# Kernel optimization log

Measured on AMD Instinct MI355X. Metric: run time of the kernel, lower is better.

Reference implementation:

```python
import jax, jax.numpy as jnp
import numpy as np

HIDDEN = 1024
HEADS = 16
HEAD_DIM = HIDDEN // HEADS  # 64
B, S = 4, 2048


def setup_inputs() -> dict:
    key = jax.random.key(0)
    ks = jax.random.split(key, 8)
    scale = 1.0 / np.sqrt(HIDDEN)
    return {
        "hidden_states": jax.random.normal(ks[0], (B, S, HIDDEN), dtype=jnp.float32),
        "attention_mask": jnp.zeros((B, S), dtype=jnp.float32),  # additive mask: 0 = keep
        "Wq": jax.random.normal(ks[1], (HIDDEN, HIDDEN), dtype=jnp.float32) * scale,
        "bq": jnp.zeros((HIDDEN,), dtype=jnp.float32),
        "Wk": jax.random.normal(ks[2], (HIDDEN, HIDDEN), dtype=jnp.float32) * scale,
        "bk": jnp.zeros((HIDDEN,), dtype=jnp.float32),
        "Wv": jax.random.normal(ks[3], (HIDDEN, HIDDEN), dtype=jnp.float32) * scale,
        "bv": jnp.zeros((HIDDEN,), dtype=jnp.float32),
    }


def reference(hidden_states, attention_mask, Wq, bq, Wk, bk, Wv, bv):
    b, s, _ = hidden_states.shape

    def split_heads(x):  # [b,s,hidden] -> [b,h,s,d]
        return x.reshape(b, s, HEADS, HEAD_DIM).transpose(0, 2, 1, 3)

    q = split_heads(hidden_states @ Wq + bq)
    k = split_heads(hidden_states @ Wk + bk)
    v = split_heads(hidden_states @ Wv + bv)

    # [b,h,s,s] attention scores, scaled, with additive mask broadcast to [b,1,1,s]
    scores = jnp.einsum("bhqd,bhkd->bhqk", q, k) / np.sqrt(HEAD_DIM)
    scores = scores + attention_mask[:, None, None, :]
    probs = jax.nn.softmax(scores, axis=-1)
    # dropout prob = 0 (eval); head_mask=None
    ctx = jnp.einsum("bhqk,bhkd->bhqd", probs, v)  # [b,h,s,d]
    return ctx.transpose(0, 2, 1, 3).reshape(b, s, HIDDEN)
```

## Files before the change

### kernel.cpp

```cpp
#include <hip/hip_runtime.h>
#include <hip/hip_bf16.h>

typedef unsigned short u16t;
typedef unsigned int   u32t;
typedef float  f32x4  __attribute__((ext_vector_type(4)));
typedef __bf16 bf16x8 __attribute__((ext_vector_type(8)));

#define HIDDEN 1024
#define HEADS  16
#define HDIM   64
#define BB     4
#define SS     2048
#define BH     (BB * HEADS)
#define MTOT   (BB * SS)

__device__ inline u16t f2bf(float f) {
  __hip_bfloat16 h = __float2bfloat16(f);
  return *reinterpret_cast<u16t*>(&h);
}

__device__ inline void gload_lds16(const void* g, void* l) {
  __builtin_amdgcn_global_load_lds(
      (const __attribute__((address_space(1))) void*)g,
      (__attribute__((address_space(3))) void*)l, 16, 0, 0);
}

__global__ __launch_bounds__(256) void k_convert_x(const float* __restrict__ X,
                                                   u16t* __restrict__ Xb, int n4) {
  int i = blockIdx.x * blockDim.x + threadIdx.x;
  int stride = gridDim.x * blockDim.x;
  for (; i < n4; i += stride) {
    float4 v = reinterpret_cast<const float4*>(X)[i];
    ushort4 o;
    o.x = f2bf(v.x); o.y = f2bf(v.y); o.z = f2bf(v.z); o.w = f2bf(v.w);
    reinterpret_cast<ushort4*>(Xb)[i] = o;
  }
}

__global__ __launch_bounds__(256) void k_transpose_w(const float* __restrict__ Wq,
                                                     const float* __restrict__ Wk,
                                                     const float* __restrict__ Wv,
                                                     u16t* __restrict__ Wt) {
  __shared__ float tile[64][65];
  const int mat = blockIdx.z;
  const float* W = (mat == 0) ? Wq : (mat == 1) ? Wk : Wv;
  const int k0 = blockIdx.x * 64, n0 = blockIdx.y * 64;
  const int t = threadIdx.x;
  const int c = t & 63, rbase = t >> 6;
#pragma unroll
  for (int p = 0; p < 16; ++p) {
    int r = p * 4 + rbase;
    tile[r][c] = W[(size_t)(k0 + r) * HIDDEN + n0 + c];
  }
  __syncthreads();
  u16t* Wo = Wt + (size_t)mat * HIDDEN * HIDDEN;
#pragma unroll
  for (int p = 0; p < 16; ++p) {
    int r = p * 4 + rbase;
    Wo[(size_t)(n0 + r) * HIDDEN + k0 + c] = f2bf(tile[c][r]);
  }
}

__global__ __launch_bounds__(256) void k_qkv_gemm(const u16t* __restrict__ Xb,
                                                  const u16t* __restrict__ Wt,
                                                  const float* __restrict__ bq,
                                                  const float* __restrict__ bk,
                                                  const float* __restrict__ bv,
                                                  u16t* __restrict__ QKV) {
  __shared__ __align__(16) u16t As[128 * 64];
  __shared__ __align__(16) u16t Bs[128 * 64];
  const int m0 = blockIdx.x * 128, n0 = blockIdx.y * 128;
  const int tid = threadIdx.x;
  const int w = tid >> 6, l = tid & 63;
  const int lq = l & 15, g = l >> 4;
  const int wm = (w >> 1) * 64, wn = (w & 1) * 64;

  f32x4 acc[4][4] = {};

  for (int t = 0; t < 16; ++t) {
    const int k0 = t * 64;
    __syncthreads();
#pragma unroll
    for (int p = 0; p < 4; ++p) {
      int chunk = p * 256 + tid;
      int row = chunk >> 3, c16 = chunk & 7;
      int sc = ((c16 ^ (row & 7)) * 8);
      gload_lds16(Xb + (size_t)(m0 + row) * HIDDEN + k0 + sc,
                  &As[(p * 256 + w * 64) * 8]);
      gload_lds16(Wt + (size_t)(n0 + row) * HIDDEN + k0 + sc,
                  &Bs[(p * 256 + w * 64) * 8]);
    }
    __syncthreads();
#pragma unroll
    for (int kc = 0; kc < 2; ++kc) {
      bf16x8 af[4], bfr[4];
#pragma unroll
      for (int i = 0; i < 4; ++i) {
        int rowA = wm + i * 16 + lq;
        af[i] = *reinterpret_cast<const bf16x8*>(
            &As[rowA * 64 + (((kc * 4 + g) ^ (rowA & 7)) * 8)]);
        int rowB = wn + i * 16 + lq;
        bfr[i] = *reinterpret_cast<const bf16x8*>(
            &Bs[rowB * 64 + (((kc * 4 + g) ^ (rowB & 7)) * 8)]);
      }
#pragma unroll
      for (int i = 0; i < 4; ++i)
#pragma unroll
        for (int j = 0; j < 4; ++j)
          acc[i][j] = __builtin_amdgcn_mfma_f32_16x16x32_bf16(af[i], bfr[j],
                                                              acc[i][j], 0, 0, 0);
    }
  }

  const int nb = n0 >> 10;
  const float* bias = (nb == 0) ? bq : (nb == 1) ? bk : bv;
  const float scl = (nb == 0) ? 0.125f : 1.0f;
#pragma unroll
  for (int j = 0; j < 4; ++j) {
    int n = (n0 & 1023) + wn + j * 16 + lq;
    int h = n >> 6, d = n & 63;
    float bval = bias[n];
#pragma unroll
    for (int i = 0; i < 4; ++i) {
#pragma unroll
      for (int r = 0; r < 4; ++r) {
        int m = m0 + wm + i * 16 + g * 4 + r;
        int b = m >> 11, s = m & 2047;
        QKV[(((size_t)(nb * BH + b * HEADS + h)) * SS + s) * HDIM + d] =
            f2bf((acc[i][j][r] + bval) * scl);
      }
    }
  }
}

__global__ __launch_bounds__(256) void k_attn(const u16t* __restrict__ QKV,
                                              const float* __restrict__ mask,
                                              float* __restrict__ out) {
  __shared__ __align__(16) u16t Ks[64 * 64];
  __shared__ __align__(16) u16t Vt[64 * 64];
  const int qt = blockIdx.x, bh = blockIdx.y;
  const int b = bh >> 4, h = bh & 15;
  const int tid = threadIdx.x, w = tid >> 6, l = tid & 63;
  const int lq = l & 15, g = l >> 4;
  const int q0 = qt * 128 + w * 32;

  const u16t* Qh = QKV + (size_t)bh * SS * HDIM;
  const u16t* Kh = QKV + (size_t)(BH + bh) * SS * HDIM;
  const u16t* Vh = QKV + (size_t)(2 * BH + bh) * SS * HDIM;

  bf16x8 qf[2][2];
#pragma unroll
  for (int qi = 0; qi < 2; ++qi) {
    qf[qi][0] = *reinterpret_cast<const bf16x8*>(
        &Qh[(size_t)(q0 + qi * 16 + lq) * HDIM + g * 8]);
    qf[qi][1] = *reinterpret_cast<const bf16x8*>(
        &Qh[(size_t)(q0 + qi * 16 + lq) * HDIM + 32 + g * 8]);
  }

  float m_run[2] = {-1e30f, -1e30f};
  float lsum[2] = {0.f, 0.f};
  f32x4 ctx[2][4] = {};

  const int srcl1 = ((2 * g) & 3) * 16 + lq;
  const int srcl2 = ((2 * g + 1) & 3) * 16 + lq;
  const bool hi = (g >= 2);

  for (int kv = 0; kv < 32; ++kv) {
    const int k0 = kv * 64;
    __syncthreads();
#pragma unroll
    for (int p = 0; p < 2; ++p) {
      int chunk = p * 256 + tid;
      int row = chunk >> 3, c16 = chunk & 7;
      gload_lds16(Kh + (size_t)(k0 + row) * HDIM + ((c16 ^ (row & 7)) * 8),
                  &Ks[(p * 256 + w * 64) * 8]);
    }
#pragma unroll
    for (int p = 0; p < 2; ++p) {
      int chunk = p * 256 + tid;
      int vrow = chunk >> 3, c8 = chunk & 7;
      bf16x8 v = *reinterpret_cast<const bf16x8*>(
          &Vh[(size_t)(k0 + vrow) * HDIM + c8 * 8]);
      const u16t* vv = reinterpret_cast<const u16t*>(&v);
#pragma unroll
      for (int jj = 0; jj < 8; ++jj) {
        int d = c8 * 8 + jj;
        int sc = ((((vrow >> 3) + (d >> 3)) & 7) ^ (d & 7));
        Vt[d * 64 + sc * 8 + (vrow & 7)] = vv[jj];
      }
    }
    __syncthreads();

    bf16x8 kf[4][2];
#pragma unroll
    for (int mt = 0; mt < 4; ++mt) {
      int row = mt * 16 + lq;
      kf[mt][0] = *reinterpret_cast<const bf16x8*>(
          &Ks[row * 64 + ((g ^ (row & 7)) * 8)]);
      kf[mt][1] = *reinterpret_cast<const bf16x8*>(
          &Ks[row * 64 + (((4 + g) ^ (row & 7)) * 8)]);
    }

    u32t pk[2][4][2];
#pragma unroll
    for (int qi = 0; qi < 2; ++qi) {
      f32x4 s[4];
#pragma unroll
      for (int mt = 0; mt < 4; ++mt) {
        f32x4 z = {};
        z = __builtin_amdgcn_mfma_f32_16x16x32_bf16(kf[mt][0], qf[qi][0], z, 0, 0, 0);
        z = __builtin_amdgcn_mfma_f32_16x16x32_bf16(kf[mt][1], qf[qi][1], z, 0, 0, 0);
        const float4 mv = *reinterpret_cast<const float4*>(
            &mask[b * SS + k0 + mt * 16 + g * 4]);
        s[mt][0] = z[0] + mv.x; s[mt][1] = z[1] + mv.y;
        s[mt][2] = z[2] + mv.z; s[mt][3] = z[3] + mv.w;
      }
      float tmax = s[0][0];
#pragma unroll
      for (int mt = 0; mt < 4; ++mt)
#pragma unroll
        for (int r = 0; r < 4; ++r) tmax = fmaxf(tmax, s[mt][r]);
      tmax = fmaxf(tmax, __shfl_xor(tmax, 16));
      tmax = fmaxf(tmax, __shfl_xor(tmax, 32));
      float mn = fmaxf(m_run[qi], tmax);
      float sc = __expf(m_run[qi] - mn);
      m_run[qi] = mn;
      float ps = 0.f;
#pragma unroll
      for (int mt = 0; mt < 4; ++mt) {
        float p0 = __expf(s[mt][0] - mn), p1 = __expf(s[mt][1] - mn);
        float p2 = __expf(s[mt][2] - mn), p3 = __expf(s[mt][3] - mn);
        ps += (p0 + p1) + (p2 + p3);
        pk[qi][mt][0] = ((u32t)f2bf(p1) << 16) | f2bf(p0);
        pk[qi][mt][1] = ((u32t)f2bf(p3) << 16) | f2bf(p2);
      }
      lsum[qi] = lsum[qi] * sc + ps;
#pragma unroll
      for (int dt = 0; dt < 4; ++dt) {
        ctx[qi][dt][0] *= sc; ctx[qi][dt][1] *= sc;
        ctx[qi][dt][2] *= sc; ctx[qi][dt][3] *= sc;
      }
    }

#pragma unroll
    for (int c = 0; c < 2; ++c) {
      bf16x8 pb[2];
#pragma unroll
      for (int qi = 0; qi < 2; ++qi) {
        u32t w0a = (u32t)__shfl((int)pk[qi][c * 2][0], srcl1);
        u32t w0b = (u32t)__shfl((int)pk[qi][c * 2 + 1][0], srcl1);
        u32t w1a = (u32t)__shfl((int)pk[qi][c * 2][1], srcl1);
        u32t w1b = (u32t)__shfl((int)pk[qi][c * 2 + 1][1], srcl1);
        u32t w2a = (u32t)__shfl((int)pk[qi][c * 2][0], srcl2);
        u32t w2b = (u32t)__shfl((int)pk[qi][c * 2 + 1][0], srcl2);
        u32t w3a = (u32t)__shfl((int)pk[qi][c * 2][1], srcl2);
        u32t w3b = (u32t)__shfl((int)pk[qi][c * 2 + 1][1], srcl2);
        union { u32t u[4]; bf16x8 v; } uu;
        uu.u[0] = hi ? w0b : w0a;
        uu.u[1] = hi ? w1b : w1a;
        uu.u[2] = hi ? w2b : w2a;
        uu.u[3] = hi ? w3b : w3a;
        pb[qi] = uu.v;
      }
#pragma unroll
      for (int dt = 0; dt < 4; ++dt) {
        int d = dt * 16 + lq;
        int cc = c * 4 + g;
        int scn = (((cc + (d >> 3)) & 7) ^ (d & 7));
        bf16x8 vf = *reinterpret_cast<const bf16x8*>(&Vt[d * 64 + scn * 8]);
        ctx[0][dt] = __builtin_amdgcn_mfma_f32_16x16x32_bf16(vf, pb[0], ctx[0][dt], 0, 0, 0);
        ctx[1][dt] = __builtin_amdgcn_mfma_f32_16x16x32_bf16(vf, pb[1], ctx[1][dt], 0, 0, 0);
      }
    }
  }

#pragma unroll
  for (int qi = 0; qi < 2; ++qi) {
    float ls = lsum[qi];
    ls += __shfl_xor(ls, 16);
    ls += __shfl_xor(ls, 32);
    float rinv = 1.0f / ls;
    int qg = q0 + qi * 16 + lq;
#pragma unroll
    for (int dt = 0; dt < 4; ++dt) {
      float4 o;
      o.x = ctx[qi][dt][0] * rinv; o.y = ctx[qi][dt][1] * rinv;
      o.z = ctx[qi][dt][2] * rinv; o.w = ctx[qi][dt][3] * rinv;
      *reinterpret_cast<float4*>(
          &out[((size_t)(b * SS + qg)) * HIDDEN + h * HDIM + dt * 16 + g * 4]) = o;
    }
  }
}

extern "C" void kernel_launch(void* const* d_in, const int* in_sizes, int n_in,
                              void* d_out, int out_size, void* d_ws, size_t ws_size,
                              hipStream_t stream) {
  const float* X    = (const float*)d_in[0];
  const float* mask = (const float*)d_in[1];
  const float* Wq   = (const float*)d_in[2];
  const float* bq   = (const float*)d_in[3];
  const float* Wk   = (const float*)d_in[4];
  const float* bk   = (const float*)d_in[5];
  const float* Wv   = (const float*)d_in[6];
  const float* bv   = (const float*)d_in[7];
  float* out = (float*)d_out;

  u16t* Xb  = (u16t*)d_ws;
  u16t* Wt  = Xb + (size_t)MTOT * HIDDEN;
  u16t* QKV = Wt + (size_t)3 * HIDDEN * HIDDEN;

  hipLaunchKernelGGL(k_convert_x, dim3(2048), dim3(256), 0, stream,
                     X, Xb, MTOT * HIDDEN / 4);
  hipLaunchKernelGGL(k_transpose_w, dim3(16, 16, 3), dim3(256), 0, stream,
                     Wq, Wk, Wv, Wt);
  hipLaunchKernelGGL(k_qkv_gemm, dim3(MTOT / 128, 3 * HIDDEN / 128), dim3(256), 0, stream,
                     Xb, Wt, bq, bk, bv, QKV);
  hipLaunchKernelGGL(k_attn, dim3(SS / 128, BH), dim3(256), 0, stream,
                     QKV, mask, out);
}
```

Before: 327.6 us.

## Double-buffer K/V in attention, pre-transpose V in GEMM, use exp2 with lazy rescale

```diff
diff --git a/kernel.cpp b/kernel.cpp
--- a/kernel.cpp
+++ b/kernel.cpp
@@ -13,10 +13,19 @@
 #define SS     2048
 #define BH     (BB * HEADS)
 #define MTOT   (BB * SS)
+#define LOG2E  1.4426950408889634f
 
 __device__ inline u16t f2bf(float f) {
   __hip_bfloat16 h = __float2bfloat16(f);
   return *reinterpret_cast<u16t*>(&h);
+}
+
+__device__ inline float fast_exp2(float x) {
+#if __has_builtin(__builtin_amdgcn_exp2f)
+  return __builtin_amdgcn_exp2f(x);
+#else
+  return exp2f(x);
+#endif
 }
 
 __device__ inline void gload_lds16(const void* g, void* l) {
@@ -61,15 +70,17 @@
   }
 }
 
+template <bool SWAP>
 __global__ __launch_bounds__(256) void k_qkv_gemm(const u16t* __restrict__ Xb,
                                                   const u16t* __restrict__ Wt,
                                                   const float* __restrict__ bq,
                                                   const float* __restrict__ bk,
                                                   const float* __restrict__ bv,
-                                                  u16t* __restrict__ QKV) {
+                                                  u16t* __restrict__ QKV,
+                                                  int n0base) {
   __shared__ __align__(16) u16t As[128 * 64];
   __shared__ __align__(16) u16t Bs[128 * 64];
-  const int m0 = blockIdx.x * 128, n0 = blockIdx.y * 128;
+  const int m0 = blockIdx.x * 128, n0 = n0base + blockIdx.y * 128;
   const int tid = threadIdx.x;
   const int w = tid >> 6, l = tid & 63;
   const int lq = l & 15, g = l >> 4;
@@ -106,28 +117,59 @@
 #pragma unroll
       for (int i = 0; i < 4; ++i)
 #pragma unroll
-        for (int j = 0; j < 4; ++j)
-          acc[i][j] = __builtin_amdgcn_mfma_f32_16x16x32_bf16(af[i], bfr[j],
-                                                              acc[i][j], 0, 0, 0);
-    }
-  }
-
-  const int nb = n0 >> 10;
-  const float* bias = (nb == 0) ? bq : (nb == 1) ? bk : bv;
-  const float scl = (nb == 0) ? 0.125f : 1.0f;
-#pragma unroll
-  for (int j = 0; j < 4; ++j) {
-    int n = (n0 & 1023) + wn + j * 16 + lq;
-    int h = n >> 6, d = n & 63;
-    float bval = bias[n];
-#pragma unroll
-    for (int i = 0; i < 4; ++i) {
-#pragma unroll
-      for (int r = 0; r < 4; ++r) {
-        int m = m0 + wm + i * 16 + g * 4 + r;
+        for (int j = 0; j < 4; ++j) {
+          if constexpr (SWAP)
+            acc[i][j] = __builtin_amdgcn_mfma_f32_16x16x32_bf16(bfr[j], af[i],
+                                                                acc[i][j], 0, 0, 0);
+          else
+            acc[i][j] = __builtin_amdgcn_mfma_f32_16x16x32_bf16(af[i], bfr[j],
+                                                                acc[i][j], 0, 0, 0);
+        }
+    }
+  }
+
+  if constexpr (SWAP) {
+    const int nb_ = n0 >> 10;
+    const float* bias = nb_ ? bk : bq;
+    const float scl = nb_ ? 1.0f : 0.125f * LOG2E;
+#pragma unroll
+    for (int j = 0; j < 4; ++j) {
+      int nf = (n0 & 1023) + wn + j * 16 + g * 4;
+      int h = nf >> 6, d0 = nf & 63;
+      float4 b4 = *reinterpret_cast<const float4*>(&bias[nf]);
+#pragma unroll
+      for (int i = 0; i < 4; ++i) {
+        int m = m0 + wm + i * 16 + lq;
         int b = m >> 11, s = m & 2047;
-        QKV[(((size_t)(nb * BH + b * HEADS + h)) * SS + s) * HDIM + d] =
-            f2bf((acc[i][j][r] + bval) * scl);
+        ushort4 o;
+        o.x = f2bf((acc[i][j][0] + b4.x) * scl);
+        o.y = f2bf((acc[i][j][1] + b4.y) * scl);
+        o.z = f2bf((acc[i][j][2] + b4.z) * scl);
+        o.w = f2bf((acc[i][j][3] + b4.w) * scl);
+        *reinterpret_cast<ushort4*>(
+            &QKV[(((size_t)(nb_ * BH + b * HEADS + h)) * SS + s) * HDIM + d0]) = o;
+      }
+    }
+  } else {
+    u16t* Vg = QKV + (size_t)2 * BH * SS * HDIM;
+#pragma unroll
+    for (int j = 0; j < 4; ++j) {
+      int n = (n0 - 2048) + wn + j * 16 + lq;
+      int h = n >> 6, d = n & 63;
+      float bval = bv[n];
+#pragma unroll
+      for (int i = 0; i < 4; ++i) {
+        int m = m0 + wm + i * 16 + g * 4;
+        int b = m >> 11, s = m & 2047;
+        int tt = s >> 6, k = s & 63;
+        int slot = (k & 32) + ((k >> 2) & 3) * 8 + ((k >> 4) & 1) * 4;
+        ushort4 o;
+        o.x = f2bf(acc[i][j][0] + bval);
+        o.y = f2bf(acc[i][j][1] + bval);
+        o.z = f2bf(acc[i][j][2] + bval);
+        o.w = f2bf(acc[i][j][3] + bval);
+        *reinterpret_cast<ushort4*>(
+            &Vg[(((size_t)(b * HEADS + h)) * HDIM + d) * SS + tt * 64 + slot]) = o;
       }
     }
   }
@@ -136,8 +178,9 @@
 __global__ __launch_bounds__(256) void k_attn(const u16t* __restrict__ QKV,
                                               const float* __restrict__ mask,
                                               float* __restrict__ out) {
-  __shared__ __align__(16) u16t Ks[64 * 64];
-  __shared__ __align__(16) u16t Vt[64 * 64];
+  __shared__ __align__(16) u16t Ks[2][64 * 64];
+  __shared__ __align__(16) u16t Vs[2][64 * 64];
+  __shared__ float Ms[SS];
   const int qt = blockIdx.x, bh = blockIdx.y;
   const int b = bh >> 4, h = bh & 15;
   const int tid = threadIdx.x, w = tid >> 6, l = tid & 63;
@@ -146,7 +189,17 @@
 
   const u16t* Qh = QKV + (size_t)bh * SS * HDIM;
   const u16t* Kh = QKV + (size_t)(BH + bh) * SS * HDIM;
-  const u16t* Vh = QKV + (size_t)(2 * BH + bh) * SS * HDIM;
+  const u16t* Vh = QKV + (size_t)(2 * BH) * SS * HDIM + (size_t)bh * HDIM * SS;
+
+  {
+    const float4* m4 = reinterpret_cast<const float4*>(mask + (size_t)b * SS);
+    float4* s4 = reinterpret_cast<float4*>(Ms);
+    for (int i = tid; i < SS / 4; i += 256) {
+      float4 v = m4[i];
+      v.x *= LOG2E; v.y *= LOG2E; v.z *= LOG2E; v.w *= LOG2E;
+      s4[i] = v;
+    }
+  }
 
   bf16x8 qf[2][2];
 #pragma unroll
@@ -157,64 +210,66 @@
         &Qh[(size_t)(q0 + qi * 16 + lq) * HDIM + 32 + g * 8]);
   }
 
+  const int cA = tid, cB = 256 + tid;
+  const u16t* ksrcA = Kh + (size_t)(cA >> 3) * HDIM + (((cA & 7) ^ ((cA >> 3) & 7)) * 8);
+  const u16t* ksrcB = Kh + (size_t)(cB >> 3) * HDIM + (((cB & 7) ^ ((cB >> 3) & 7)) * 8);
+  const u16t* vsrcA = Vh + (size_t)(cA >> 3) * SS + (((cA & 7) ^ ((cA >> 3) & 7)) * 8);
+  const u16t* vsrcB = Vh + (size_t)(cB >> 3) * SS + (((cB & 7) ^ ((cB >> 3) & 7)) * 8);
+
+  auto STAGE = [&](int t, int bufi) {
+    const size_t ko = (size_t)t * 64 * HDIM;
+    const int vo = t * 64;
+    gload_lds16(ksrcA + ko, &Ks[bufi][(w * 64) * 8]);
+    gload_lds16(ksrcB + ko, &Ks[bufi][(256 + w * 64) * 8]);
+    gload_lds16(vsrcA + vo, &Vs[bufi][(w * 64) * 8]);
+    gload_lds16(vsrcB + vo, &Vs[bufi][(256 + w * 64) * 8]);
+  };
+
   float m_run[2] = {-1e30f, -1e30f};
   float lsum[2] = {0.f, 0.f};
   f32x4 ctx[2][4] = {};
-
-  const int srcl1 = ((2 * g) & 3) * 16 + lq;
-  const int srcl2 = ((2 * g + 1) & 3) * 16 + lq;
-  const bool hi = (g >= 2);
+  u32t pk[2][4][2];
+
+  STAGE(0, 0);
+  __syncthreads();
 
   for (int kv = 0; kv < 32; ++kv) {
+    const int cur = kv & 1;
     const int k0 = kv * 64;
-    __syncthreads();
-#pragma unroll
-    for (int p = 0; p < 2; ++p) {
-      int chunk = p * 256 + tid;
-      int row = chunk >> 3, c16 = chunk & 7;
-      gload_lds16(Kh + (size_t)(k0 + row) * HDIM + ((c16 ^ (row & 7)) * 8),
-                  &Ks[(p * 256 + w * 64) * 8]);
-    }
-#pragma unroll
-    for (int p = 0; p < 2; ++p) {
-      int chunk = p * 256 + tid;
-      int vrow = chunk >> 3, c8 = chunk & 7;
-      bf16x8 v = *reinterpret_cast<const bf16x8*>(
-          &Vh[(size_t)(k0 + vrow) * HDIM + c8 * 8]);
-      const u16t* vv = reinterpret_cast<const u16t*>(&v);
-#pragma unroll
-      for (int jj = 0; jj < 8; ++jj) {
-        int d = c8 * 8 + jj;
-        int sc = ((((vrow >> 3) + (d >> 3)) & 7) ^ (d & 7));
-        Vt[d * 64 + sc * 8 + (vrow & 7)] = vv[jj];
-      }
-    }
-    __syncthreads();
+    STAGE((kv + 1) & 31, cur ^ 1);
+    asm volatile("s_waitcnt vmcnt(4)\n\ts_barrier" ::: "memory");
+
+    const u16t* Kb = &Ks[cur][0];
+    const u16t* Vb = &Vs[cur][0];
 
     bf16x8 kf[4][2];
 #pragma unroll
     for (int mt = 0; mt < 4; ++mt) {
       int row = mt * 16 + lq;
       kf[mt][0] = *reinterpret_cast<const bf16x8*>(
-          &Ks[row * 64 + ((g ^ (row & 7)) * 8)]);
+          &Kb[row * 64 + ((g ^ (row & 7)) * 8)]);
       kf[mt][1] = *reinterpret_cast<const bf16x8*>(
-          &Ks[row * 64 + (((4 + g) ^ (row & 7)) * 8)]);
-    }
-
-    u32t pk[2][4][2];
+          &Kb[row * 64 + (((4 + g) ^ (row & 7)) * 8)]);
+    }
+
+    float4 mvs[4];
+#pragma unroll
+    for (int mt = 0; mt < 4; ++mt)
+      mvs[mt] = *reinterpret_cast<const float4*>(&Ms[k0 + mt * 16 + g * 4]);
+
 #pragma unroll
     for (int qi = 0; qi < 2; ++qi) {
       f32x4 s[4];
+      __builtin_amdgcn_s_setprio(1);
 #pragma unroll
       for (int mt = 0; mt < 4; ++mt) {
         f32x4 z = {};
         z = __builtin_amdgcn_mfma_f32_16x16x32_bf16(kf[mt][0], qf[qi][0], z, 0, 0, 0);
         z = __builtin_amdgcn_mfma_f32_16x16x32_bf16(kf[mt][1], qf[qi][1], z, 0, 0, 0);
-        const float4 mv = *reinterpret_cast<const float4*>(
-            &mask[b * SS + k0 + mt * 16 + g * 4]);
-        s[mt][0] = z[0] + mv.x; s[mt][1] = z[1] + mv.y;
-        s[mt][2] = z[2] + mv.z; s[mt][3] = z[3] + mv.w;
-      }
+        s[mt][0] = z[0] + mvs[mt].x; s[mt][1] = z[1] + mvs[mt].y;
+        s[mt][2] = z[2] + mvs[mt].z; s[mt][3] = z[3] + mvs[mt].w;
+      }
+      __builtin_amdgcn_s_setprio(0);
       float tmax = s[0][0];
 #pragma unroll
       for (int mt = 0; mt < 4; ++mt)
@@ -222,56 +277,53 @@
         for (int r = 0; r < 4; ++r) tmax = fmaxf(tmax, s[mt][r]);
       tmax = fmaxf(tmax, __shfl_xor(tmax, 16));
       tmax = fmaxf(tmax, __shfl_xor(tmax, 32));
-      float mn = fmaxf(m_run[qi], tmax);
-      float sc = __expf(m_run[qi] - mn);
-      m_run[qi] = mn;
+      if (__any(tmax > m_run[qi] + 8.f)) {
+        float nm = fmaxf(m_run[qi], tmax);
+        float sc = fast_exp2(m_run[qi] - nm);
+        m_run[qi] = nm;
+        lsum[qi] *= sc;
+#pragma unroll
+        for (int dt = 0; dt < 4; ++dt) {
+          ctx[qi][dt][0] *= sc; ctx[qi][dt][1] *= sc;
+          ctx[qi][dt][2] *= sc; ctx[qi][dt][3] *= sc;
+        }
+      }
+      const float mn = m_run[qi];
       float ps = 0.f;
 #pragma unroll
       for (int mt = 0; mt < 4; ++mt) {
-        float p0 = __expf(s[mt][0] - mn), p1 = __expf(s[mt][1] - mn);
-        float p2 = __expf(s[mt][2] - mn), p3 = __expf(s[mt][3] - mn);
+        float p0 = fast_exp2(s[mt][0] - mn), p1 = fast_exp2(s[mt][1] - mn);
+        float p2 = fast_exp2(s[mt][2] - mn), p3 = fast_exp2(s[mt][3] - mn);
         ps += (p0 + p1) + (p2 + p3);
         pk[qi][mt][0] = ((u32t)f2bf(p1) << 16) | f2bf(p0);
         pk[qi][mt][1] = ((u32t)f2bf(p3) << 16) | f2bf(p2);
       }
-      lsum[qi] = lsum[qi] * sc + ps;
-#pragma unroll
-      for (int dt = 0; dt < 4; ++dt) {
-        ctx[qi][dt][0] *= sc; ctx[qi][dt][1] *= sc;
-        ctx[qi][dt][2] *= sc; ctx[qi][dt][3] *= sc;
-      }
+      lsum[qi] += ps;
     }
 
 #pragma unroll
     for (int c = 0; c < 2; ++c) {
-      bf16x8 pb[2];
+      union { u32t u[4]; bf16x8 v; } pb[2];
 #pragma unroll
       for (int qi = 0; qi < 2; ++qi) {
-        u32t w0a = (u32t)__shfl((int)pk[qi][c * 2][0], srcl1);
-        u32t w0b = (u32t)__shfl((int)pk[qi][c * 2 + 1][0], srcl1);
-        u32t w1a = (u32t)__shfl((int)pk[qi][c * 2][1], srcl1);
-        u32t w1b = (u32t)__shfl((int)pk[qi][c * 2 + 1][1], srcl1);
-        u32t w2a = (u32t)__shfl((int)pk[qi][c * 2][0], srcl2);
-        u32t w2b = (u32t)__shfl((int)pk[qi][c * 2 + 1][0], srcl2);
-        u32t w3a = (u32t)__shfl((int)pk[qi][c * 2][1], srcl2);
-        u32t w3b = (u32t)__shfl((int)pk[qi][c * 2 + 1][1], srcl2);
-        union { u32t u[4]; bf16x8 v; } uu;
-        uu.u[0] = hi ? w0b : w0a;
-        uu.u[1] = hi ? w1b : w1a;
-        uu.u[2] = hi ? w2b : w2a;
-        uu.u[3] = hi ? w3b : w3a;
-        pb[qi] = uu.v;
-      }
+        pb[qi].u[0] = pk[qi][2 * c][0];
+        pb[qi].u[1] = pk[qi][2 * c][1];
+        pb[qi].u[2] = pk[qi][2 * c + 1][0];
+        pb[qi].u[3] = pk[qi][2 * c + 1][1];
+      }
+      __builtin_amdgcn_s_setprio(1);
 #pragma unroll
       for (int dt = 0; dt < 4; ++dt) {
         int d = dt * 16 + lq;
-        int cc = c * 4 + g;
-        int scn = (((cc + (d >> 3)) & 7) ^ (d & 7));
-        bf16x8 vf = *reinterpret_cast<const bf16x8*>(&Vt[d * 64 + scn * 8]);
-        ctx[0][dt] = __builtin_amdgcn_mfma_f32_16x16x32_bf16(vf, pb[0], ctx[0][dt], 0, 0, 0);
-        ctx[1][dt] = __builtin_amdgcn_mfma_f32_16x16x32_bf16(vf, pb[1], ctx[1][dt], 0, 0, 0);
-      }
-    }
+        bf16x8 vf = *reinterpret_cast<const bf16x8*>(
+            &Vb[d * 64 + (((4 * c + g) ^ (d & 7)) * 8)]);
+        ctx[0][dt] = __builtin_amdgcn_mfma_f32_16x16x32_bf16(vf, pb[0].v, ctx[0][dt], 0, 0, 0);
+        ctx[1][dt] = __builtin_amdgcn_mfma_f32_16x16x32_bf16(vf, pb[1].v, ctx[1][dt], 0, 0, 0);
+      }
+      __builtin_amdgcn_s_setprio(0);
+    }
+
+    asm volatile("s_barrier" ::: "memory");
   }
 
 #pragma unroll
@@ -313,8 +365,10 @@
                      X, Xb, MTOT * HIDDEN / 4);
   hipLaunchKernelGGL(k_transpose_w, dim3(16, 16, 3), dim3(256), 0, stream,
                      Wq, Wk, Wv, Wt);
-  hipLaunchKernelGGL(k_qkv_gemm, dim3(MTOT / 128, 3 * HIDDEN / 128), dim3(256), 0, stream,
-                     Xb, Wt, bq, bk, bv, QKV);
+  hipLaunchKernelGGL((k_qkv_gemm<true>), dim3(MTOT / 128, 16), dim3(256), 0, stream,
+                     Xb, Wt, bq, bk, bv, QKV, 0);
+  hipLaunchKernelGGL((k_qkv_gemm<false>), dim3(MTOT / 128, 8), dim3(256), 0, stream,
+                     Xb, Wt, bq, bk, bv, QKV, 2048);
   hipLaunchKernelGGL(k_attn, dim3(SS / 128, BH), dim3(256), 0, stream,
                      QKV, mask, out);
 }
```

Result: faster. 299.0 us (-8.8%).
